# Optimization experiments

Hardware: AMD Instinct MI355X
Metric: run time of the kernel (lower is better)

## Reference

```python
import jax, jax.numpy as jnp
import numpy as np

N_NODES = 100000
N_FEAT = 128
HIDDEN = 64
OUT = 16
N_EDGES = 3200000
N_POS = 500000
N_NEG = 500000


def setup_inputs() -> dict:
    key = jax.random.key(0)
    ks = jax.random.split(key, 8)
    x = jax.random.normal(ks[0], (N_NODES, N_FEAT), dtype=jnp.float32)
    edge_index = jax.random.randint(ks[1], (2, N_EDGES), 0, N_NODES, dtype=jnp.int64)
    pos_edge_index = jax.random.randint(ks[2], (2, N_POS), 0, N_NODES, dtype=jnp.int64)
    neg_edge_index = jax.random.randint(ks[3], (2, N_NEG), 0, N_NODES, dtype=jnp.int64)
    W1 = jax.random.normal(ks[4], (N_FEAT, HIDDEN), dtype=jnp.float32) * (1.0 / np.sqrt(N_FEAT))
    b1 = jnp.zeros((HIDDEN,), dtype=jnp.float32)
    W2 = jax.random.normal(ks[5], (HIDDEN, OUT), dtype=jnp.float32) * (1.0 / np.sqrt(HIDDEN))
    b2 = jnp.zeros((OUT,), dtype=jnp.float32)
    return {"x": x, "edge_index": edge_index, "pos_edge_index": pos_edge_index,
            "neg_edge_index": neg_edge_index, "W1": W1, "b1": b1, "W2": W2, "b2": b2}


def gcn_conv(x, W, b, src, dst):
    """PyG GCNConv with add_self_loops=True: D^-1/2 (A+I) D^-1/2 X W + b."""
    n = x.shape[0]
    h = x @ W  # [N, out]
    # degree including self-loop (+1)
    deg = jax.ops.segment_sum(jnp.ones(dst.shape, dtype=h.dtype), dst, num_segments=n) + 1.0
    dis = jax.lax.rsqrt(deg)  # deg >= 1, never inf
    coef = dis[src] * dis[dst]  # [E]
    agg = jax.ops.segment_sum(h[src] * coef[:, None], dst, num_segments=n)
    # self-loop message: norm = dis[i]*dis[i]
    agg = agg + h * (dis * dis)[:, None]
    return agg + b


def reference(x, edge_index, pos_edge_index, neg_edge_index, W1, b1, W2, b2):
    src, dst = edge_index[0], edge_index[1]
    z = jax.nn.relu(gcn_conv(x, W1, b1, src, dst))
    z = gcn_conv(z, W2, b2, src, dst)  # [N, 16]
    ei = jnp.concatenate([pos_edge_index, neg_edge_index], axis=-1)  # [2, P+Q]
    logits = jnp.sum(z[ei[0]] * z[ei[1]], axis=-1)  # [P+Q]
    return logits
```

## Files before the change

### kernel.cpp

```cpp
#include <hip/hip_runtime.h>

#define F 128
#define H 64
#define O 16

#define BSHIFT 7
#define BSZ 128
#define NSUB 8
#define SUBCAP 768
#define ACHUNK 8192
#define XS 136

typedef _Float16 half8_t __attribute__((ext_vector_type(8)));
typedef _Float16 half4_t __attribute__((ext_vector_type(4)));
typedef float f32x4 __attribute__((ext_vector_type(4)));

__global__ void k_bcur2(int* __restrict__ bcur, int NC) {
    int i = blockIdx.x * blockDim.x + threadIdx.x;
    if (i < NC) bcur[i] = i * SUBCAP;
}

__global__ __launch_bounds__(512) void k_bucketA(const int* __restrict__ src,
                                                 const int* __restrict__ dstv,
                                                 int* __restrict__ bcur,
                                                 int* __restrict__ bdata, int E) {
    __shared__ int hist[1024];
    for (int t = threadIdx.x; t < 1024; t += 512) hist[t] = 0;
    __syncthreads();
    int base = blockIdx.x * ACHUNK;
    int end = min(base + ACHUNK, E);
    for (int i = base + threadIdx.x; i < end; i += 512) {
        atomicAdd(&hist[dstv[i] >> BSHIFT], 1);
    }
    __syncthreads();
    int sub = blockIdx.x & (NSUB - 1);
    for (int b = threadIdx.x; b < 1024; b += 512) {
        int c = hist[b];
        if (c > 0) hist[b] = atomicAdd(&bcur[b * NSUB + sub], c);
    }
    __syncthreads();
    for (int i = base + threadIdx.x; i < end; i += 512) {
        int d = dstv[i];
        int b = d >> BSHIFT;
        int pos = atomicAdd(&hist[b], 1);
        bdata[pos] = (src[i] << BSHIFT) | (d & (BSZ - 1));
    }
}

__global__ __launch_bounds__(256) void k_bdeg(const int* __restrict__ bdata,
                                              const int* __restrict__ bcur,
                                              int* __restrict__ deg,
                                              float* __restrict__ dis, int N) {
    __shared__ int h[BSZ];
    int b = blockIdx.x;
    int node0 = b << BSHIFT;
    int nloc = min(BSZ, N - node0);
    for (int t = threadIdx.x; t < BSZ; t += 256) h[t] = 0;
    __syncthreads();
    for (int s = 0; s < NSUB; s++) {
        int start = (b * NSUB + s) * SUBCAP;
        int end = bcur[b * NSUB + s];
        for (int p = start + threadIdx.x; p < end; p += 256)
            atomicAdd(&h[bdata[p] & (BSZ - 1)], 1);
    }
    __syncthreads();
    for (int t = threadIdx.x; t < nloc; t += 256) {
        int d = h[t];
        deg[node0 + t] = d;
        dis[node0 + t] = rsqrtf((float)d + 1.0f);
    }
}

__global__ void k_bscan(const int* __restrict__ bcur, int* __restrict__ bstart, int NBK) {
    __shared__ int s[1024];
    int tid = threadIdx.x;
    int tot = 0;
    if (tid < NBK) {
        for (int ss = 0; ss < NSUB; ss++)
            tot += bcur[tid * NSUB + ss] - (tid * NSUB + ss) * SUBCAP;
    }
    s[tid] = tot;
    __syncthreads();
    for (int off = 1; off < 1024; off <<= 1) {
        int v = (tid >= off) ? s[tid - off] : 0;
        __syncthreads();
        s[tid] += v;
        __syncthreads();
    }
    bstart[tid] = s[tid] - tot;
}

__global__ __launch_bounds__(256) void k_bplace(const int* __restrict__ bdata,
                                                const int* __restrict__ bcur,
                                                const int* __restrict__ deg,
                                                const int* __restrict__ bstart,
                                                int* __restrict__ row_ptr,
                                                int* __restrict__ col, int N) {
    __shared__ int pref[BSZ];
    __shared__ int cur[BSZ];
    int b = blockIdx.x;
    int node0 = b << BSHIFT;
    int nloc = min(BSZ, N - node0);
    int tid = threadIdx.x;
    int myDeg = 0;
    if (tid < BSZ) {
        myDeg = (tid < nloc) ? deg[node0 + tid] : 0;
        pref[tid] = myDeg;
    }
    __syncthreads();
    for (int off = 1; off < BSZ; off <<= 1) {
        int v = (tid < BSZ && tid >= off) ? pref[tid - off] : 0;
        __syncthreads();
        if (tid < BSZ) pref[tid] += v;
        __syncthreads();
    }
    int base = bstart[b];
    if (tid < nloc) {
        int excl = base + pref[tid] - myDeg;
        cur[tid] = excl;
        row_ptr[node0 + tid] = excl;
    }
    if (tid == 0) row_ptr[node0 + nloc] = base + pref[BSZ - 1];
    __syncthreads();
    for (int s = 0; s < NSUB; s++) {
        int start = (b * NSUB + s) * SUBCAP;
        int end = bcur[b * NSUB + s];
        for (int p = start + tid; p < end; p += 256) {
            int v = bdata[p];
            int pos = atomicAdd(&cur[v & (BSZ - 1)], 1);
            col[pos] = v >> BSHIFT;
        }
    }
}

__global__ void k_wprep(const float* __restrict__ W1, _Float16* __restrict__ wt_hi,
                        _Float16* __restrict__ wt_lo) {
    int idx = blockIdx.x * 256 + threadIdx.x;
    int c = idx >> 7, k = idx & 127;
    float w = W1[k * H + c];
    _Float16 hi = (_Float16)w;
    wt_hi[idx] = hi;
    wt_lo[idx] = (_Float16)(w - (float)hi);
}

__global__ __launch_bounds__(256) void k_gemm1(const float* __restrict__ x,
                                               const _Float16* __restrict__ wt_hi,
                                               const _Float16* __restrict__ wt_lo,
                                               const float* __restrict__ dis,
                                               _Float16* __restrict__ h1p, int N) {
    __shared__ _Float16 xh[64 * XS], xl[64 * XS], wh[64 * XS], wl[64 * XS];
    int tid = threadIdx.x;
    int row0 = blockIdx.x * 64;
#pragma unroll
    for (int i = 0; i < 8; i++) {
        int idx = i * 256 + tid;
        int r = idx >> 5;
        int c = (idx & 31) * 4;
        int rr = row0 + r; if (rr >= N) rr = N - 1;
        float4 v = *(const float4*)(x + (size_t)rr * F + c);
        half4_t h = {(_Float16)v.x, (_Float16)v.y, (_Float16)v.z, (_Float16)v.w};
        half4_t l = {(_Float16)(v.x - (float)h[0]), (_Float16)(v.y - (float)h[1]),
                     (_Float16)(v.z - (float)h[2]), (_Float16)(v.w - (float)h[3])};
        *(half4_t*)(xh + r * XS + c) = h;
        *(half4_t*)(xl + r * XS + c) = l;
    }
#pragma unroll
    for (int i = 0; i < 4; i++) {
        int idx = i * 256 + tid;
        int c = idx >> 4;
        int k8 = (idx & 15) * 8;
        *(half8_t*)(wh + c * XS + k8) = *(const half8_t*)(wt_hi + c * 128 + k8);
        *(half8_t*)(wl + c * XS + k8) = *(const half8_t*)(wt_lo + c * 128 + k8);
    }
    __syncthreads();
    int wv = tid >> 6, lane = tid & 63;
    int m = lane & 15, qd = lane >> 4;
    const _Float16* xhp = xh + (wv * 16 + m) * XS;
    const _Float16* xlp = xl + (wv * 16 + m) * XS;
    f32x4 acc[4] = {f32x4{0,0,0,0}, f32x4{0,0,0,0}, f32x4{0,0,0,0}, f32x4{0,0,0,0}};
#pragma unroll
    for (int kc = 0; kc < 4; kc++) {
        int ko = kc * 32 + qd * 8;
        half8_t ah = *(const half8_t*)(xhp + ko);
        half8_t al = *(const half8_t*)(xlp + ko);
#pragma unroll
        for (int nt = 0; nt < 4; nt++) {
            half8_t bh = *(const half8_t*)(wh + (nt * 16 + m) * XS + ko);
            half8_t bl = *(const half8_t*)(wl + (nt * 16 + m) * XS + ko);
            acc[nt] = __builtin_amdgcn_mfma_f32_16x16x32_f16(ah, bh, acc[nt], 0, 0, 0);
            acc[nt] = __builtin_amdgcn_mfma_f32_16x16x32_f16(ah, bl, acc[nt], 0, 0, 0);
            acc[nt] = __builtin_amdgcn_mfma_f32_16x16x32_f16(al, bh, acc[nt], 0, 0, 0);
        }
    }
#pragma unroll
    for (int reg = 0; reg < 4; reg++) {
        int row = row0 + wv * 16 + qd * 4 + reg;
        if (row < N) {
            float d = dis[row];
#pragma unroll
            for (int nt = 0; nt < 4; nt++) {
                h1p[(size_t)row * H + nt * 16 + m] = (_Float16)(acc[nt][reg] * d);
            }
        }
    }
}

__global__ __launch_bounds__(256) void k_gather1(const _Float16* __restrict__ h1p,
                                                 const float* __restrict__ dis,
                                                 const int* __restrict__ row_ptr,
                                                 const int* __restrict__ col,
                                                 const float* __restrict__ b1,
                                                 float* __restrict__ z, int N) {
    int node = blockIdx.x * 4 + (threadIdx.x >> 6);
    if (node >= N) return;
    int lane = threadIdx.x & 63;
    int g = lane >> 3;
    int t = lane & 7;
    const half8_t* hp = (const half8_t*)h1p;
    float acc[8];
#pragma unroll
    for (int j = 0; j < 8; j++) acc[j] = 0.f;
    int e = row_ptr[node + 1];
    int p = row_ptr[node] + g;
    for (; p + 8 < e; p += 16) {
        int s0 = col[p], s1 = col[p + 8];
        half8_t v0 = hp[(size_t)s0 * 8 + t];
        half8_t v1 = hp[(size_t)s1 * 8 + t];
#pragma unroll
        for (int j = 0; j < 8; j++) acc[j] += (float)v0[j];
#pragma unroll
        for (int j = 0; j < 8; j++) acc[j] += (float)v1[j];
    }
    if (p < e) {
        int s0 = col[p];
        half8_t v0 = hp[(size_t)s0 * 8 + t];
#pragma unroll
        for (int j = 0; j < 8; j++) acc[j] += (float)v0[j];
    }
#pragma unroll
    for (int off = 8; off < 64; off <<= 1) {
#pragma unroll
        for (int j = 0; j < 8; j++) acc[j] += __shfl_xor(acc[j], off);
    }
    if (g == 0) {
        float dn = dis[node];
        half8_t self = hp[(size_t)node * 8 + t];
        float o[8];
#pragma unroll
        for (int j = 0; j < 8; j++)
            o[j] = fmaxf(fmaf(acc[j] + (float)self[j], dn, b1[t * 8 + j]), 0.f);
        float4* zp = (float4*)(z + (size_t)node * H + t * 8);
        zp[0] = float4{o[0], o[1], o[2], o[3]};
        zp[1] = float4{o[4], o[5], o[6], o[7]};
    }
}

__global__ __launch_bounds__(64) void k_gemm2(const float* __restrict__ z,
                                              const float* __restrict__ W2,
                                              const float* __restrict__ dis,
                                              _Float16* __restrict__ h2p, int N) {
    __shared__ float zs[64 * 65];
    int lane = threadIdx.x;
    int row0 = blockIdx.x * 64;
#pragma unroll
    for (int i = 0; i < 16; i++) {
        int r = i * 4 + (lane >> 4);
        int c = (lane & 15) * 4;
        int rr = row0 + r; if (rr >= N) rr = N - 1;
        float4 v = *(const float4*)(z + (size_t)rr * H + c);
        zs[r * 65 + c + 0] = v.x;
        zs[r * 65 + c + 1] = v.y;
        zs[r * 65 + c + 2] = v.z;
        zs[r * 65 + c + 3] = v.w;
    }
    __syncthreads();
    float acc[O];
#pragma unroll
    for (int c = 0; c < O; c++) acc[c] = 0.f;
#pragma unroll 4
    for (int k = 0; k < H; k++) {
        float a = zs[lane * 65 + k];
        const float* wrow = W2 + (size_t)k * O;
#pragma unroll
        for (int c = 0; c < O; c++) acc[c] = fmaf(a, wrow[c], acc[c]);
    }
    int row = row0 + lane;
    if (row < N) {
        float d = dis[row];
        half8_t* orow = (half8_t*)(h2p + (size_t)row * O);
#pragma unroll
        for (int c0 = 0; c0 < O; c0 += 8) {
            half8_t o;
#pragma unroll
            for (int j = 0; j < 8; j++) o[j] = (_Float16)(acc[c0 + j] * d);
            orow[c0 / 8] = o;
        }
    }
}

__global__ __launch_bounds__(256) void k_gather2(const _Float16* __restrict__ h2p,
                                                 const float* __restrict__ dis,
                                                 const int* __restrict__ row_ptr,
                                                 const int* __restrict__ col,
                                                 const float* __restrict__ b2,
                                                 float* __restrict__ z2, int N) {
    int node = blockIdx.x * 4 + (threadIdx.x >> 6);
    if (node >= N) return;
    int lane = threadIdx.x & 63;
    int g = lane >> 1;
    int t = lane & 1;
    const half8_t* hp = (const half8_t*)h2p;
    float acc[8];
#pragma unroll
    for (int j = 0; j < 8; j++) acc[j] = 0.f;
    int e = row_ptr[node + 1];
    for (int p = row_ptr[node] + g; p < e; p += 32) {
        int s = col[p];
        half8_t v = hp[(size_t)s * 2 + t];
#pragma unroll
        for (int j = 0; j < 8; j++) acc[j] += (float)v[j];
    }
#pragma unroll
    for (int off = 2; off < 64; off <<= 1) {
#pragma unroll
        for (int j = 0; j < 8; j++) acc[j] += __shfl_xor(acc[j], off);
    }
    if (g == 0) {
        float dn = dis[node];
        half8_t self = hp[(size_t)node * 2 + t];
        float o[8];
#pragma unroll
        for (int j = 0; j < 8; j++)
            o[j] = fmaf(acc[j] + (float)self[j], dn, b2[t * 8 + j]);
        float4* zp = (float4*)(z2 + (size_t)node * O + t * 8);
        zp[0] = float4{o[0], o[1], o[2], o[3]};
        zp[1] = float4{o[4], o[5], o[6], o[7]};
    }
}

__global__ __launch_bounds__(256) void k_logits(const float* __restrict__ z2,
                                                const int* __restrict__ pos,
                                                const int* __restrict__ neg,
                                                float* __restrict__ out, int P, int Q) {
    int tid = blockIdx.x * 256 + threadIdx.x;
    int i = tid >> 2;
    if (i >= P + Q) return;
    int k = tid & 3;
    int a, b;
    if (i < P) { a = pos[i]; b = pos[P + i]; }
    else       { int t = i - P; a = neg[t]; b = neg[Q + t]; }
    float4 va = *(const float4*)(z2 + (size_t)a * O + k * 4);
    float4 vb = *(const float4*)(z2 + (size_t)b * O + k * 4);
    float r = va.x * vb.x + va.y * vb.y + va.z * vb.z + va.w * vb.w;
    r += __shfl_xor(r, 1);
    r += __shfl_xor(r, 2);
    if (k == 0) out[i] = r;
}

extern "C" void kernel_launch(void* const* d_in, const int* in_sizes, int n_in,
                              void* d_out, int out_size, void* d_ws, size_t ws_size,
                              hipStream_t stream) {
    const float* x   = (const float*)d_in[0];
    const int*   ei  = (const int*)d_in[1];
    const int*   pos = (const int*)d_in[2];
    const int*   neg = (const int*)d_in[3];
    const float* W1  = (const float*)d_in[4];
    const float* b1  = (const float*)d_in[5];
    const float* W2  = (const float*)d_in[6];
    const float* b2  = (const float*)d_in[7];
    float* out = (float*)d_out;

    int N = in_sizes[0] / F;
    int E = in_sizes[1] / 2;
    int P = in_sizes[2] / 2;
    int Q = in_sizes[3] / 2;
    const int* src  = ei;
    const int* dstv = ei + E;

    int Npad = ((N + 255) / 256) * 256;
    int Epad = (E + 63) & ~63;
    int NBK = (N + BSZ - 1) / BSZ;
    int NC  = NBK * NSUB;

    char* w = (char*)d_ws;
    int*      deg   = (int*)w;        w += (size_t)Npad * 4;
    float*    dis   = (float*)w;      w += (size_t)Npad * 4;
    int*      row_ptr = (int*)w;      w += (size_t)(Npad + 256) * 4;
    int*      bcur  = (int*)w;        w += 8192 * 4;
    int*      bstart = (int*)w;       w += 1024 * 4;
    int*      col   = (int*)w;        w += (size_t)Epad * 4;
    _Float16* h1p   = (_Float16*)w;
    int*      bdata = (int*)w;
    size_t h1b = (size_t)N * H * 2, bdb = (size_t)NC * SUBCAP * 4;
    w += (h1b > bdb ? h1b : bdb);
    float*    z     = (float*)w;      w += (size_t)N * H * 4;
    _Float16* h2p   = (_Float16*)w;   w += (size_t)N * O * 2;
    float*    z2    = (float*)w;      w += (size_t)N * O * 4;
    _Float16* wt_hi = (_Float16*)w;   w += (size_t)H * F * 2;
    _Float16* wt_lo = (_Float16*)w;

    k_wprep<<<(H * F + 255) / 256, 256, 0, stream>>>(W1, wt_hi, wt_lo);
    k_bcur2<<<(NC + 255) / 256, 256, 0, stream>>>(bcur, NC);
    k_bucketA<<<(E + ACHUNK - 1) / ACHUNK, 512, 0, stream>>>(src, dstv, bcur, bdata, E);
    k_bdeg<<<NBK, 256, 0, stream>>>(bdata, bcur, deg, dis, N);
    k_bscan<<<1, 1024, 0, stream>>>(bcur, bstart, NBK);
    k_bplace<<<NBK, 256, 0, stream>>>(bdata, bcur, deg, bstart, row_ptr, col, N);

    k_gemm1<<<(N + 63) / 64, 256, 0, stream>>>(x, wt_hi, wt_lo, dis, h1p, N);
    k_gather1<<<(N + 3) / 4, 256, 0, stream>>>(h1p, dis, row_ptr, col, b1, z, N);

    k_gemm2<<<(N + 63) / 64, 64, 0, stream>>>(z, W2, dis, h2p, N);
    k_gather2<<<(N + 3) / 4, 256, 0, stream>>>(h2p, dis, row_ptr, col, b2, z2, N);

    k_logits<<<((P + Q) * 4 + 255) / 256, 256, 0, stream>>>(z2, pos, neg, out, P, Q);
}
```

Measured before the change: 330.5 us.

## Fuse GEMM2 into gather1, merge degree pass into bplace, vectorize bucketing

Layer 2's small GEMM (64x16) now runs inside gather1 using a transposed W2 held in shared memory. This removes the fp32 z intermediate (N*64 floats written and read back) and the k_gemm2 launch. The degree histogram and rsqrt move into k_bplace, the W1 prep merges with the bcur init, and bucketA reads src/dst with int4 loads. NSUB is doubled while SUBCAP is halved, which spreads global atomic contention but leaves less headroom per sub-bucket before overflow.

New measurement: 328.1 us. No clear change (-0.7%).

```diff
diff --git a/kernel.cpp b/kernel.cpp
--- a/kernel.cpp
+++ b/kernel.cpp
@@ -6,8 +6,8 @@
 
 #define BSHIFT 7
 #define BSZ 128
-#define NSUB 8
-#define SUBCAP 768
+#define NSUB 16
+#define SUBCAP 384
 #define ACHUNK 8192
 #define XS 136
 
@@ -15,9 +15,17 @@
 typedef _Float16 half4_t __attribute__((ext_vector_type(4)));
 typedef float f32x4 __attribute__((ext_vector_type(4)));
 
-__global__ void k_bcur2(int* __restrict__ bcur, int NC) {
+__global__ void k_prep(const float* __restrict__ W1, _Float16* __restrict__ wt_hi,
+                       _Float16* __restrict__ wt_lo, int* __restrict__ bcur, int NC) {
     int i = blockIdx.x * blockDim.x + threadIdx.x;
     if (i < NC) bcur[i] = i * SUBCAP;
+    if (i < H * F) {
+        int c = i >> 7, k = i & 127;
+        float w = W1[k * H + c];
+        _Float16 hi = (_Float16)w;
+        wt_hi[i] = hi;
+        wt_lo[i] = (_Float16)(w - (float)hi);
+    }
 }
 
 __global__ __launch_bounds__(512) void k_bucketA(const int* __restrict__ src,
@@ -29,45 +37,39 @@
     __syncthreads();
     int base = blockIdx.x * ACHUNK;
     int end = min(base + ACHUNK, E);
-    for (int i = base + threadIdx.x; i < end; i += 512) {
+    int tid = threadIdx.x;
+    for (int i = base + tid * 4; i + 3 < end; i += 2048) {
+        int4 d4 = *(const int4*)(dstv + i);
+        atomicAdd(&hist[d4.x >> BSHIFT], 1);
+        atomicAdd(&hist[d4.y >> BSHIFT], 1);
+        atomicAdd(&hist[d4.z >> BSHIFT], 1);
+        atomicAdd(&hist[d4.w >> BSHIFT], 1);
+    }
+    for (int i = base + ((end - base) & ~3) + tid; i < end; i += 512)
         atomicAdd(&hist[dstv[i] >> BSHIFT], 1);
-    }
     __syncthreads();
     int sub = blockIdx.x & (NSUB - 1);
-    for (int b = threadIdx.x; b < 1024; b += 512) {
+    for (int b = tid; b < 1024; b += 512) {
         int c = hist[b];
         if (c > 0) hist[b] = atomicAdd(&bcur[b * NSUB + sub], c);
     }
     __syncthreads();
-    for (int i = base + threadIdx.x; i < end; i += 512) {
+    for (int i = base + tid * 4; i + 3 < end; i += 2048) {
+        int4 s4 = *(const int4*)(src + i);
+        int4 d4 = *(const int4*)(dstv + i);
+        int p0 = atomicAdd(&hist[d4.x >> BSHIFT], 1);
+        bdata[p0] = (s4.x << BSHIFT) | (d4.x & (BSZ - 1));
+        int p1 = atomicAdd(&hist[d4.y >> BSHIFT], 1);
+        bdata[p1] = (s4.y << BSHIFT) | (d4.y & (BSZ - 1));
+        int p2 = atomicAdd(&hist[d4.z >> BSHIFT], 1);
+        bdata[p2] = (s4.z << BSHIFT) | (d4.z & (BSZ - 1));
+        int p3 = atomicAdd(&hist[d4.w >> BSHIFT], 1);
+        bdata[p3] = (s4.w << BSHIFT) | (d4.w & (BSZ - 1));
+    }
+    for (int i = base + ((end - base) & ~3) + tid; i < end; i += 512) {
         int d = dstv[i];
-        int b = d >> BSHIFT;
-        int pos = atomicAdd(&hist[b], 1);
+        int pos = atomicAdd(&hist[d >> BSHIFT], 1);
         bdata[pos] = (src[i] << BSHIFT) | (d & (BSZ - 1));
-    }
-}
-
-__global__ __launch_bounds__(256) void k_bdeg(const int* __restrict__ bdata,
-                                              const int* __restrict__ bcur,
-                                              int* __restrict__ deg,
-                                              float* __restrict__ dis, int N) {
-    __shared__ int h[BSZ];
-    int b = blockIdx.x;
-    int node0 = b << BSHIFT;
-    int nloc = min(BSZ, N - node0);
-    for (int t = threadIdx.x; t < BSZ; t += 256) h[t] = 0;
-    __syncthreads();
-    for (int s = 0; s < NSUB; s++) {
-        int start = (b * NSUB + s) * SUBCAP;
-        int end = bcur[b * NSUB + s];
-        for (int p = start + threadIdx.x; p < end; p += 256)
-            atomicAdd(&h[bdata[p] & (BSZ - 1)], 1);
-    }
-    __syncthreads();
-    for (int t = threadIdx.x; t < nloc; t += 256) {
-        int d = h[t];
-        deg[node0 + t] = d;
-        dis[node0 + t] = rsqrtf((float)d + 1.0f);
     }
 }
 
@@ -92,19 +94,29 @@
 
 __global__ __launch_bounds__(256) void k_bplace(const int* __restrict__ bdata,
                                                 const int* __restrict__ bcur,
-                                                const int* __restrict__ deg,
                                                 const int* __restrict__ bstart,
                                                 int* __restrict__ row_ptr,
+                                                float* __restrict__ dis,
                                                 int* __restrict__ col, int N) {
+    __shared__ int h[BSZ];
     __shared__ int pref[BSZ];
     __shared__ int cur[BSZ];
     int b = blockIdx.x;
     int node0 = b << BSHIFT;
     int nloc = min(BSZ, N - node0);
     int tid = threadIdx.x;
+    if (tid < BSZ) h[tid] = 0;
+    __syncthreads();
+    for (int s = 0; s < NSUB; s++) {
+        int start = (b * NSUB + s) * SUBCAP;
+        int end = bcur[b * NSUB + s];
+        for (int p = start + tid; p < end; p += 256)
+            atomicAdd(&h[bdata[p] & (BSZ - 1)], 1);
+    }
+    __syncthreads();
     int myDeg = 0;
     if (tid < BSZ) {
-        myDeg = (tid < nloc) ? deg[node0 + tid] : 0;
+        myDeg = h[tid];
         pref[tid] = myDeg;
     }
     __syncthreads();
@@ -119,6 +131,7 @@
         int excl = base + pref[tid] - myDeg;
         cur[tid] = excl;
         row_ptr[node0 + tid] = excl;
+        dis[node0 + tid] = rsqrtf((float)myDeg + 1.0f);
     }
     if (tid == 0) row_ptr[node0 + nloc] = base + pref[BSZ - 1];
     __syncthreads();
@@ -131,16 +144,6 @@
             col[pos] = v >> BSHIFT;
         }
     }
-}
-
-__global__ void k_wprep(const float* __restrict__ W1, _Float16* __restrict__ wt_hi,
-                        _Float16* __restrict__ wt_lo) {
-    int idx = blockIdx.x * 256 + threadIdx.x;
-    int c = idx >> 7, k = idx & 127;
-    float w = W1[k * H + c];
-    _Float16 hi = (_Float16)w;
-    wt_hi[idx] = hi;
-    wt_lo[idx] = (_Float16)(w - (float)hi);
 }
 
 __global__ __launch_bounds__(256) void k_gemm1(const float* __restrict__ x,
@@ -210,90 +213,74 @@
                                                  const int* __restrict__ row_ptr,
                                                  const int* __restrict__ col,
                                                  const float* __restrict__ b1,
-                                                 float* __restrict__ z, int N) {
-    int node = blockIdx.x * 4 + (threadIdx.x >> 6);
-    if (node >= N) return;
-    int lane = threadIdx.x & 63;
+                                                 const float* __restrict__ W2,
+                                                 _Float16* __restrict__ h2p, int N) {
+    __shared__ float w2t[16 * 65];
+    int tid = threadIdx.x;
+    {
+        int idx = tid * 4;
+        float4 v = *(const float4*)(W2 + idx);
+        const float* vp = (const float*)&v;
+#pragma unroll
+        for (int i = 0; i < 4; i++) {
+            int e = idx + i;
+            w2t[(e & 15) * 65 + (e >> 4)] = vp[i];
+        }
+    }
+    __syncthreads();
+    int node = blockIdx.x * 4 + (tid >> 6);
+    int lane = tid & 63;
     int g = lane >> 3;
     int t = lane & 7;
-    const half8_t* hp = (const half8_t*)h1p;
-    float acc[8];
-#pragma unroll
-    for (int j = 0; j < 8; j++) acc[j] = 0.f;
-    int e = row_ptr[node + 1];
-    int p = row_ptr[node] + g;
-    for (; p + 8 < e; p += 16) {
-        int s0 = col[p], s1 = col[p + 8];
-        half8_t v0 = hp[(size_t)s0 * 8 + t];
-        half8_t v1 = hp[(size_t)s1 * 8 + t];
-#pragma unroll
-        for (int j = 0; j < 8; j++) acc[j] += (float)v0[j];
-#pragma unroll
-        for (int j = 0; j < 8; j++) acc[j] += (float)v1[j];
-    }
-    if (p < e) {
-        int s0 = col[p];
-        half8_t v0 = hp[(size_t)s0 * 8 + t];
-#pragma unroll
-        for (int j = 0; j < 8; j++) acc[j] += (float)v0[j];
-    }
-#pragma unroll
-    for (int off = 8; off < 64; off <<= 1) {
-#pragma unroll
-        for (int j = 0; j < 8; j++) acc[j] += __shfl_xor(acc[j], off);
-    }
-    if (g == 0) {
+    if (node < N) {
+        const half8_t* hp = (const half8_t*)h1p;
+        float acc[8];
+#pragma unroll
+        for (int j = 0; j < 8; j++) acc[j] = 0.f;
+        int e = row_ptr[node + 1];
+        int p = row_ptr[node] + g;
+        for (; p + 8 < e; p += 16) {
+            int s0 = col[p], s1 = col[p + 8];
+            half8_t v0 = hp[(size_t)s0 * 8 + t];
+            half8_t v1 = hp[(size_t)s1 * 8 + t];
+#pragma unroll
+            for (int j = 0; j < 8; j++) acc[j] += (float)v0[j];
+#pragma unroll
+            for (int j = 0; j < 8; j++) acc[j] += (float)v1[j];
+        }
+        if (p < e) {
+            int s0 = col[p];
+            half8_t v0 = hp[(size_t)s0 * 8 + t];
+#pragma unroll
+            for (int j = 0; j < 8; j++) acc[j] += (float)v0[j];
+        }
+#pragma unroll
+        for (int off = 8; off < 64; off <<= 1) {
+#pragma unroll
+            for (int j = 0; j < 8; j++) acc[j] += __shfl_xor(acc[j], off);
+        }
         float dn = dis[node];
         half8_t self = hp[(size_t)node * 8 + t];
         float o[8];
 #pragma unroll
         for (int j = 0; j < 8; j++)
             o[j] = fmaxf(fmaf(acc[j] + (float)self[j], dn, b1[t * 8 + j]), 0.f);
-        float4* zp = (float4*)(z + (size_t)node * H + t * 8);
-        zp[0] = float4{o[0], o[1], o[2], o[3]};
-        zp[1] = float4{o[4], o[5], o[6], o[7]};
-    }
-}
-
-__global__ __launch_bounds__(64) void k_gemm2(const float* __restrict__ z,
-                                              const float* __restrict__ W2,
-                                              const float* __restrict__ dis,
-                                              _Float16* __restrict__ h2p, int N) {
-    __shared__ float zs[64 * 65];
-    int lane = threadIdx.x;
-    int row0 = blockIdx.x * 64;
-#pragma unroll
-    for (int i = 0; i < 16; i++) {
-        int r = i * 4 + (lane >> 4);
-        int c = (lane & 15) * 4;
-        int rr = row0 + r; if (rr >= N) rr = N - 1;
-        float4 v = *(const float4*)(z + (size_t)rr * H + c);
-        zs[r * 65 + c + 0] = v.x;
-        zs[r * 65 + c + 1] = v.y;
-        zs[r * 65 + c + 2] = v.z;
-        zs[r * 65 + c + 3] = v.w;
-    }
-    __syncthreads();
-    float acc[O];
-#pragma unroll
-    for (int c = 0; c < O; c++) acc[c] = 0.f;
-#pragma unroll 4
-    for (int k = 0; k < H; k++) {
-        float a = zs[lane * 65 + k];
-        const float* wrow = W2 + (size_t)k * O;
-#pragma unroll
-        for (int c = 0; c < O; c++) acc[c] = fmaf(a, wrow[c], acc[c]);
-    }
-    int row = row0 + lane;
-    if (row < N) {
-        float d = dis[row];
-        half8_t* orow = (half8_t*)(h2p + (size_t)row * O);
-#pragma unroll
-        for (int c0 = 0; c0 < O; c0 += 8) {
-            half8_t o;
-#pragma unroll
-            for (int j = 0; j < 8; j++) o[j] = (_Float16)(acc[c0 + j] * d);
-            orow[c0 / 8] = o;
+        const float* w1r = w2t + g * 65 + t * 8;
+        const float* w2r = w2t + (g + 8) * 65 + t * 8;
+        float p1 = 0.f, p2 = 0.f;
+#pragma unroll
+        for (int j = 0; j < 8; j++) {
+            p1 = fmaf(o[j], w1r[j], p1);
+            p2 = fmaf(o[j], w2r[j], p2);
+        }
+#pragma unroll
+        for (int off = 1; off < 8; off <<= 1) {
+            p1 += __shfl_xor(p1, off);
+            p2 += __shfl_xor(p2, off);
+        }
+        if (t == 0) {
+            h2p[(size_t)node * O + g]     = (_Float16)(p1 * dn);
+            h2p[(size_t)node * O + g + 8] = (_Float16)(p2 * dn);
         }
     }
 }
@@ -383,34 +370,29 @@
     int NC  = NBK * NSUB;
 
     char* w = (char*)d_ws;
-    int*      deg   = (int*)w;        w += (size_t)Npad * 4;
-    float*    dis   = (float*)w;      w += (size_t)Npad * 4;
+    float*    dis     = (float*)w;    w += (size_t)Npad * 4;
     int*      row_ptr = (int*)w;      w += (size_t)(Npad + 256) * 4;
-    int*      bcur  = (int*)w;        w += 8192 * 4;
-    int*      bstart = (int*)w;       w += 1024 * 4;
-    int*      col   = (int*)w;        w += (size_t)Epad * 4;
-    _Float16* h1p   = (_Float16*)w;
-    int*      bdata = (int*)w;
+    int*      bcur    = (int*)w;      w += 16384 * 4;
+    int*      bstart  = (int*)w;      w += 1024 * 4;
+    int*      col     = (int*)w;      w += (size_t)Epad * 4;
+    _Float16* h1p     = (_Float16*)w;
+    int*      bdata   = (int*)w;
     size_t h1b = (size_t)N * H * 2, bdb = (size_t)NC * SUBCAP * 4;
     w += (h1b > bdb ? h1b : bdb);
-    float*    z     = (float*)w;      w += (size_t)N * H * 4;
-    _Float16* h2p   = (_Float16*)w;   w += (size_t)N * O * 2;
-    float*    z2    = (float*)w;      w += (size_t)N * O * 4;
-    _Float16* wt_hi = (_Float16*)w;   w += (size_t)H * F * 2;
-    _Float16* wt_lo = (_Float16*)w;
-
-    k_wprep<<<(H * F + 255) / 256, 256, 0, stream>>>(W1, wt_hi, wt_lo);
-    k_bcur2<<<(NC + 255) / 256, 256, 0, stream>>>(bcur, NC);
+    _Float16* h2p     = (_Float16*)w; w += (size_t)N * O * 2;
+    float*    z2      = (float*)w;    w += (size_t)N * O * 4;
+    _Float16* wt_hi   = (_Float16*)w; w += (size_t)H * F * 2;
+    _Float16* wt_lo   = (_Float16*)w;
+
+    int prepN = (NC > H * F) ? NC : H * F;
+
+    k_prep<<<(prepN + 255) / 256, 256, 0, stream>>>(W1, wt_hi, wt_lo, bcur, NC);
     k_bucketA<<<(E + ACHUNK - 1) / ACHUNK, 512, 0, stream>>>(src, dstv, bcur, bdata, E);
-    k_bdeg<<<NBK, 256, 0, stream>>>(bdata, bcur, deg, dis, N);
     k_bscan<<<1, 1024, 0, stream>>>(bcur, bstart, NBK);
-    k_bplace<<<NBK, 256, 0, stream>>>(bdata, bcur, deg, bstart, row_ptr, col, N);
+    k_bplace<<<NBK, 256, 0, stream>>>(bdata, bcur, bstart, row_ptr, dis, col, N);
 
     k_gemm1<<<(N + 63) / 64, 256, 0, stream>>>(x, wt_hi, wt_lo, dis, h1p, N);
-    k_gather1<<<(N + 3) / 4, 256, 0, stream>>>(h1p, dis, row_ptr, col, b1, z, N);
-
-    k_gemm2<<<(N + 63) / 64, 64, 0, stream>>>(z, W2, dis, h2p, N);
+    k_gather1<<<(N + 3) / 4, 256, 0, stream>>>(h1p, dis, row_ptr, col, b1, W2, h2p, N);
     k_gather2<<<(N + 3) / 4, 256, 0, stream>>>(h2p, dis, row_ptr, col, b2, z2, N);
-
     k_logits<<<((P + Q) * 4 + 255) / 256, 256, 0, stream>>>(z2, pos, neg, out, P, Q);
 }
```
